# Kernel tuning notes

Hardware: AMD Instinct MI355X
Metric: run time of the kernel (lower is better)

## Reference

```python
import jax, jax.numpy as jnp
import numpy as np

IMAGE_W = 640.0
IMAGE_H = 640.0
ALPHA = 0.25
GAMMA = 2.0
BETA = 1.0 / 9.0
EPS = 1e-4
FACTOR = jnp.array([0.1, 0.1, 0.2, 0.2], dtype=jnp.float32)

B, A, C, M = 8, 76725, 80, 20


def _iou(anchors, gts):
    # anchors [A,4], gts [M,4] -> [A,M]
    lt = jnp.maximum(anchors[:, None, :2], gts[None, :, :2])
    rb = jnp.minimum(anchors[:, None, 2:], gts[None, :, 2:])
    wh = jnp.clip(rb - lt, 0.0)
    inter = wh[..., 0] * wh[..., 1]
    area_a = (anchors[:, 2] - anchors[:, 0]) * (anchors[:, 3] - anchors[:, 1])
    area_g = (gts[:, 2] - gts[:, 0]) * (gts[:, 3] - gts[:, 1])
    union = area_a[:, None] + area_g[None, :] - inter
    return inter / jnp.maximum(union, 1e-6)


def _snap(gt_boxes, anchors):
    # xyxy -> (tx,ty,tw,th)/factor
    awh = anchors[:, 2:] - anchors[:, :2]
    actr = anchors[:, :2] + 0.5 * awh
    gwh = jnp.maximum(gt_boxes[:, 2:] - gt_boxes[:, :2], 1.0)
    gctr = gt_boxes[:, :2] + 0.5 * gwh
    t = jnp.concatenate([(gctr - actr) / awh, jnp.log(gwh / awh)], axis=1)
    return t / FACTOR


def _assign(anchors, ann):
    # anchors [A,4], ann [M,5] -> boxes [A,4], cls [A]
    valid = ann[:, 4] >= 0.0
    gt_boxes, gt_cls = ann[:, :4], ann[:, 4]
    ious = jnp.where(valid[None, :], _iou(anchors, gt_boxes), -1.0)
    idx = jnp.argmax(ious, axis=1)
    overlap = jnp.take_along_axis(ious, idx[:, None], axis=1)[:, 0]
    boxes = _snap(gt_boxes[idx], anchors)
    cls = jnp.full_like(overlap, -1.0)
    cls = jnp.where(overlap < 0.4, 0.0, cls)
    cls = jnp.where(overlap >= 0.5, gt_cls[idx] + 1.0, cls)
    cls = jnp.where(jnp.any(valid), cls, -1.0)  # no gt: all ignore
    return boxes, cls


def setup_inputs() -> dict:
    key = jax.random.key(0)
    k1, k2, k3, k4, k5, k6, k7 = jax.random.split(key, 7)
    ctr = jax.random.uniform(k1, (B, A, 2), minval=0.0, maxval=640.0)
    wh = jax.random.uniform(k2, (B, A, 2), minval=16.0, maxval=256.0)
    batch_anchors = jnp.concatenate([ctr - 0.5 * wh, ctr + 0.5 * wh], axis=-1)
    cls_heads = jax.random.uniform(k3, (B, A, C), minval=0.01, maxval=0.99)
    reg_heads = jax.random.normal(k4, (B, A, 4)) * 0.1
    xy = jax.random.uniform(k5, (B, M, 2), minval=0.0, maxval=480.0)
    gwh = jax.random.uniform(k6, (B, M, 2), minval=32.0, maxval=160.0)
    gcls = jax.random.randint(k7, (B, M), 0, C).astype(jnp.float32)
    gcls = gcls.at[:, 15:].set(-1.0)  # pad slots
    annotations = jnp.concatenate([xy, xy + gwh, gcls[..., None]], axis=-1)
    return {"cls_heads": cls_heads, "reg_heads": reg_heads,
            "batch_anchors": batch_anchors, "annotations": annotations}


def reference(cls_heads, reg_heads, batch_anchors, annotations):
    # border filter (original drops rows; we mask -> same loss)
    border = ((batch_anchors[..., 0] > 0.0) & (batch_anchors[..., 1] > 0.0) &
              (batch_anchors[..., 2] < IMAGE_W) & (batch_anchors[..., 3] < IMAGE_H))
    boxes, cls = jax.vmap(_assign)(batch_anchors, annotations)  # [B,A,4],[B,A]
    cls = jnp.where(border, cls, -1.0)
    pos = cls > 0.0
    keep = cls >= 0.0
    pos_num = jnp.sum(pos, axis=1)  # [B]
    valid_img = pos_num > 0
    safe_pos = jnp.maximum(pos_num, 1).astype(cls_heads.dtype)

    # focal (cls) loss
    p = jnp.clip(cls_heads, EPS, 1.0 - EPS)
    gt = jax.nn.one_hot(cls.astype(jnp.int32), C + 1, dtype=p.dtype)[..., 1:]
    af = jnp.where(gt == 1.0, ALPHA, 1.0 - ALPHA)
    pt = jnp.where(gt == 1.0, p, 1.0 - p)
    bce = -(gt * jnp.log(p) + (1.0 - gt) * jnp.log(1.0 - p))
    focal = af * (1.0 - pt) ** GAMMA * bce
    per_img_cls = jnp.sum(focal * keep[..., None].astype(p.dtype), axis=(1, 2)) / safe_pos
    per_img_cls = jnp.where(valid_img, per_img_cls, 0.0)

    # smooth-L1 (reg) loss
    x = jnp.abs(reg_heads - boxes)
    sl1 = jnp.where(x >= BETA, x - 0.5 * BETA, 0.5 * x * x / BETA).mean(axis=2)
    per_img_reg = jnp.sum(sl1 * pos.astype(sl1.dtype), axis=1) / safe_pos
    per_img_reg = jnp.where(valid_img, per_img_reg, 0.0)

    n = jnp.maximum(jnp.sum(valid_img), 1).astype(per_img_cls.dtype)
    return per_img_cls.sum() / n, per_img_reg.sum() / n
```

## Files before the change

kernel.cpp:

```cpp
#include <hip/hip_runtime.h>
#include <math.h>

#define B_CNT 8
#define A_CNT 76725
#define C_CNT 80
#define M_CNT 20

constexpr int XR = (A_CNT + 255) / 256;
constexpr int XC = 512;
constexpr int NG = (A_CNT + 15) / 16;

__global__ __launch_bounds__(256) void assign_kernel(
    const float* __restrict__ anchors,
    const float* __restrict__ reg_heads,
    const float* __restrict__ ann,
    float* __restrict__ cls_out,
    double* __restrict__ partial_reg,
    int* __restrict__ partial_pos)
{
    __shared__ float s_ann[M_CNT * 5];
    const int b   = blockIdx.y;
    const int tid = threadIdx.x;
    if (tid < M_CNT * 5) s_ann[tid] = ann[b * M_CNT * 5 + tid];
    __syncthreads();

    const int a = blockIdx.x * 256 + tid;
    double slsum = 0.0;
    int pos = 0;

    if (a < A_CNT) {
        const float4 ab = ((const float4*)anchors)[b * A_CNT + a];
        const float ax1 = ab.x, ay1 = ab.y, ax2 = ab.z, ay2 = ab.w;
        const bool border = (ax1 > 0.0f) && (ay1 > 0.0f) &&
                            (ax2 < 640.0f) && (ay2 < 640.0f);
        const float area_a = (ax2 - ax1) * (ay2 - ay1);

        float best = -INFINITY;
        int   bi   = 0;
        bool  anyv = false;
        #pragma unroll
        for (int m = 0; m < M_CNT; ++m) {
            const float gx1 = s_ann[m * 5 + 0];
            const float gy1 = s_ann[m * 5 + 1];
            const float gx2 = s_ann[m * 5 + 2];
            const float gy2 = s_ann[m * 5 + 3];
            const float gc  = s_ann[m * 5 + 4];
            const bool v = (gc >= 0.0f);
            anyv = anyv || v;
            const float ltx = fmaxf(ax1, gx1), lty = fmaxf(ay1, gy1);
            const float rbx = fminf(ax2, gx2), rby = fminf(ay2, gy2);
            const float wx = fmaxf(rbx - ltx, 0.0f);
            const float wy = fmaxf(rby - lty, 0.0f);
            const float inter = wx * wy;
            const float area_g = (gx2 - gx1) * (gy2 - gy1);
            const float uni = area_a + area_g - inter;
            const float iou = v ? (inter / fmaxf(uni, 1e-6f)) : -1.0f;
            if (iou > best) { best = iou; bi = m; }
        }

        float clsv = -1.0f;
        if (anyv) {
            if (best < 0.4f)       clsv = 0.0f;
            else if (best >= 0.5f) clsv = s_ann[bi * 5 + 4] + 1.0f;
        }
        if (!border) clsv = -1.0f;
        cls_out[b * A_CNT + a] = clsv;

        if (clsv > 0.0f) {
            pos = 1;
            const float gx1 = s_ann[bi * 5 + 0];
            const float gy1 = s_ann[bi * 5 + 1];
            const float gx2 = s_ann[bi * 5 + 2];
            const float gy2 = s_ann[bi * 5 + 3];
            const float aw = ax2 - ax1, ah = ay2 - ay1;
            const float acx = ax1 + 0.5f * aw, acy = ay1 + 0.5f * ah;
            const float gw = fmaxf(gx2 - gx1, 1.0f);
            const float gh = fmaxf(gy2 - gy1, 1.0f);
            const float gcx = gx1 + 0.5f * gw, gcy = gy1 + 0.5f * gh;
            const float t0 = ((gcx - acx) / aw) / 0.1f;
            const float t1 = ((gcy - acy) / ah) / 0.1f;
            const float t2 = logf(gw / aw) / 0.2f;
            const float t3 = logf(gh / ah) / 0.2f;
            const float4 rh = ((const float4*)reg_heads)[b * A_CNT + a];

            const float BETA = (float)(1.0 / 9.0);
            const float HB   = (float)(0.5 * (1.0 / 9.0));
            auto sl1 = [&](float x) {
                x = fabsf(x);
                return (x >= BETA) ? (x - HB) : (0.5f * x * x / BETA);
            };
            const float s = (sl1(rh.x - t0) + sl1(rh.y - t1) +
                             sl1(rh.z - t2) + sl1(rh.w - t3)) * 0.25f;
            slsum = (double)s;
        }
    }

    for (int o = 32; o; o >>= 1) {
        slsum += __shfl_down(slsum, o);
        pos   += __shfl_down(pos, o);
    }
    __shared__ double sd[4];
    __shared__ int    si[4];
    const int w = tid >> 6;
    if ((tid & 63) == 0) { sd[w] = slsum; si[w] = pos; }
    __syncthreads();
    if (tid == 0) {
        partial_reg[b * XR + blockIdx.x] = sd[0] + sd[1] + sd[2] + sd[3];
        partial_pos[b * XR + blockIdx.x] = si[0] + si[1] + si[2] + si[3];
    }
}

__global__ __launch_bounds__(320) void focal_kernel(
    const float* __restrict__ cls_heads,
    const float* __restrict__ cls_f,
    double* __restrict__ partial_cls)
{
    const int b   = blockIdx.y;
    const int tid = threadIdx.x;
    const int la  = tid / 20;
    const int c0  = (tid % 20) * 4;

    double acc = 0.0;
    for (int g = blockIdx.x; g < NG; g += XC) {
        const int a = g * 16 + la;
        if (a >= A_CNT) continue;
        const float clsv = cls_f[b * A_CNT + a];
        if (clsv < 0.0f) continue;
        const int gidx = (int)clsv - 1;

        const float4 p4 = *((const float4*)(
            cls_heads + ((size_t)b * A_CNT + (size_t)a) * C_CNT + c0));
        const float pp[4] = {p4.x, p4.y, p4.z, p4.w};

        float lacc = 0.0f;
        #pragma unroll
        for (int j = 0; j < 4; ++j) {
            const float p   = fminf(fmaxf(pp[j], 1e-4f), 0.9999f);
            const float omp = 1.0f - p;
            const bool  isgt = (c0 + j) == gidx;
            const float q  = isgt ? omp : (1.0f - omp);
            const float af = isgt ? 0.25f : 0.75f;
            const float x  = isgt ? p : omp;
            lacc += af * (q * q) * (-__logf(x));
        }
        acc += (double)lacc;
    }

    for (int o = 32; o; o >>= 1) acc += __shfl_down(acc, o);
    __shared__ double sd[5];
    if ((tid & 63) == 0) sd[tid >> 6] = acc;
    __syncthreads();
    if (tid == 0)
        partial_cls[b * XC + blockIdx.x] = sd[0] + sd[1] + sd[2] + sd[3] + sd[4];
}

__global__ __launch_bounds__(256) void finalize_kernel(
    const double* __restrict__ partial_cls,
    const double* __restrict__ partial_reg,
    const int* __restrict__ partial_pos,
    float* __restrict__ out)
{
    const int tid = threadIdx.x;
    __shared__ double sc[4], sr[4];
    __shared__ int    sp[4];

    double cls_tot = 0.0, reg_tot = 0.0;
    int nv = 0;

    for (int b = 0; b < B_CNT; ++b) {
        double cs = 0.0;
        for (int i = tid; i < XC; i += 256) cs += partial_cls[b * XC + i];
        double rs = 0.0;
        int    ps = 0;
        for (int i = tid; i < XR; i += 256) {
            rs += partial_reg[b * XR + i];
            ps += partial_pos[b * XR + i];
        }
        for (int o = 32; o; o >>= 1) {
            cs += __shfl_down(cs, o);
            rs += __shfl_down(rs, o);
            ps += __shfl_down(ps, o);
        }
        const int w = tid >> 6;
        if ((tid & 63) == 0) { sc[w] = cs; sr[w] = rs; sp[w] = ps; }
        __syncthreads();
        if (tid == 0) {
            const double c = sc[0] + sc[1] + sc[2] + sc[3];
            const double r = sr[0] + sr[1] + sr[2] + sr[3];
            const int    p = sp[0] + sp[1] + sp[2] + sp[3];
            if (p > 0) { cls_tot += c / (double)p; reg_tot += r / (double)p; ++nv; }
        }
        __syncthreads();
    }

    if (tid == 0) {
        const int n = (nv > 0) ? nv : 1;
        out[0] = (float)(cls_tot / (double)n);
        out[1] = (float)(reg_tot / (double)n);
    }
}

extern "C" void kernel_launch(void* const* d_in, const int* in_sizes, int n_in,
                              void* d_out, int out_size, void* d_ws, size_t ws_size,
                              hipStream_t stream) {
    const float* cls_heads = (const float*)d_in[0];
    const float* reg_heads = (const float*)d_in[1];
    const float* anchors   = (const float*)d_in[2];
    const float* ann       = (const float*)d_in[3];
    float* out = (float*)d_out;

    char* ws = (char*)d_ws;
    double* partial_cls = (double*)ws;
    double* partial_reg = (double*)(ws + 32768);
    int*    partial_pos = (int*)(ws + 32768 + 19200);
    float*  cls_f       = (float*)(ws + 32768 + 19200 + 9600);

    assign_kernel<<<dim3(XR, B_CNT), 256, 0, stream>>>(
        anchors, reg_heads, ann, cls_f, partial_reg, partial_pos);
    focal_kernel<<<dim3(XC, B_CNT), 320, 0, stream>>>(
        cls_heads, cls_f, partial_cls);
    finalize_kernel<<<1, 256, 0, stream>>>(
        partial_cls, partial_reg, partial_pos, out);
}
```

Measured before the change: 305.1 us.

## Fuse anchor assignment and focal loss into one per-block kernel

Merges the assignment kernel and the focal-loss kernel into one kernel. Each 256-anchor block computes its anchors' labels, keeps them in shared memory, then streams the matching contiguous cls_heads slab (256×80 floats) and adds its focal loss. This drops the global round trip of the per-anchor label array and one kernel launch. It also replaces the grid-stride focal loop with many blocks that each read a contiguous slab, and merges all three partial reductions into one pass. The cost is that the focal work now waits on the IoU loop within each block, and the block shape is fixed at 256 anchors.

```diff
diff --git a/kernel.cpp b/kernel.cpp
--- a/kernel.cpp
+++ b/kernel.cpp
@@ -7,26 +7,29 @@
 #define M_CNT 20
 
 constexpr int XR = (A_CNT + 255) / 256;
-constexpr int XC = 512;
-constexpr int NG = (A_CNT + 15) / 16;
-
-__global__ __launch_bounds__(256) void assign_kernel(
+
+__global__ __launch_bounds__(256) void fused_kernel(
+    const float* __restrict__ cls_heads,
+    const float* __restrict__ reg_heads,
     const float* __restrict__ anchors,
-    const float* __restrict__ reg_heads,
     const float* __restrict__ ann,
-    float* __restrict__ cls_out,
+    double* __restrict__ partial_cls,
     double* __restrict__ partial_reg,
     int* __restrict__ partial_pos)
 {
     __shared__ float s_ann[M_CNT * 5];
+    __shared__ float s_cls[256];
     const int b   = blockIdx.y;
     const int tid = threadIdx.x;
     if (tid < M_CNT * 5) s_ann[tid] = ann[b * M_CNT * 5 + tid];
     __syncthreads();
 
-    const int a = blockIdx.x * 256 + tid;
+    const int a0 = blockIdx.x * 256;
+    const int a  = a0 + tid;
+
     double slsum = 0.0;
-    int pos = 0;
+    int    pos   = 0;
+    float  clsv  = -1.0f;
 
     if (a < A_CNT) {
         const float4 ab = ((const float4*)anchors)[b * A_CNT + a];
@@ -58,13 +61,11 @@
             if (iou > best) { best = iou; bi = m; }
         }
 
-        float clsv = -1.0f;
         if (anyv) {
             if (best < 0.4f)       clsv = 0.0f;
             else if (best >= 0.5f) clsv = s_ann[bi * 5 + 4] + 1.0f;
         }
         if (!border) clsv = -1.0f;
-        cls_out[b * A_CNT + a] = clsv;
 
         if (clsv > 0.0f) {
             pos = 1;
@@ -94,42 +95,21 @@
             slsum = (double)s;
         }
     }
-
-    for (int o = 32; o; o >>= 1) {
-        slsum += __shfl_down(slsum, o);
-        pos   += __shfl_down(pos, o);
-    }
-    __shared__ double sd[4];
-    __shared__ int    si[4];
-    const int w = tid >> 6;
-    if ((tid & 63) == 0) { sd[w] = slsum; si[w] = pos; }
+    s_cls[tid] = clsv;
     __syncthreads();
-    if (tid == 0) {
-        partial_reg[b * XR + blockIdx.x] = sd[0] + sd[1] + sd[2] + sd[3];
-        partial_pos[b * XR + blockIdx.x] = si[0] + si[1] + si[2] + si[3];
-    }
-}
-
-__global__ __launch_bounds__(320) void focal_kernel(
-    const float* __restrict__ cls_heads,
-    const float* __restrict__ cls_f,
-    double* __restrict__ partial_cls)
-{
-    const int b   = blockIdx.y;
-    const int tid = threadIdx.x;
-    const int la  = tid / 20;
-    const int c0  = (tid % 20) * 4;
-
+
+    const float* slab = cls_heads + ((size_t)b * A_CNT + (size_t)a0) * C_CNT;
     double acc = 0.0;
-    for (int g = blockIdx.x; g < NG; g += XC) {
-        const int a = g * 16 + la;
-        if (a >= A_CNT) continue;
-        const float clsv = cls_f[b * A_CNT + a];
-        if (clsv < 0.0f) continue;
-        const int gidx = (int)clsv - 1;
-
-        const float4 p4 = *((const float4*)(
-            cls_heads + ((size_t)b * A_CNT + (size_t)a) * C_CNT + c0));
+    #pragma unroll 4
+    for (int i = 0; i < 20; ++i) {
+        const int idx = tid + (i << 8);
+        const int la  = idx / 20;
+        const int c0  = (idx - la * 20) * 4;
+        const float cv = s_cls[la];
+        if (cv < 0.0f) continue;
+        const int gidx = (int)cv - 1;
+
+        const float4 p4 = *((const float4*)(slab + (size_t)la * C_CNT + c0));
         const float pp[4] = {p4.x, p4.y, p4.z, p4.w};
 
         float lacc = 0.0f;
@@ -146,12 +126,21 @@
         acc += (double)lacc;
     }
 
-    for (int o = 32; o; o >>= 1) acc += __shfl_down(acc, o);
-    __shared__ double sd[5];
-    if ((tid & 63) == 0) sd[tid >> 6] = acc;
+    for (int o = 32; o; o >>= 1) {
+        acc   += __shfl_down(acc, o);
+        slsum += __shfl_down(slsum, o);
+        pos   += __shfl_down(pos, o);
+    }
+    __shared__ double sdc[4], sdr[4];
+    __shared__ int    sip[4];
+    const int w = tid >> 6;
+    if ((tid & 63) == 0) { sdc[w] = acc; sdr[w] = slsum; sip[w] = pos; }
     __syncthreads();
-    if (tid == 0)
-        partial_cls[b * XC + blockIdx.x] = sd[0] + sd[1] + sd[2] + sd[3] + sd[4];
+    if (tid == 0) {
+        partial_cls[b * XR + blockIdx.x] = sdc[0] + sdc[1] + sdc[2] + sdc[3];
+        partial_reg[b * XR + blockIdx.x] = sdr[0] + sdr[1] + sdr[2] + sdr[3];
+        partial_pos[b * XR + blockIdx.x] = sip[0] + sip[1] + sip[2] + sip[3];
+    }
 }
 
 __global__ __launch_bounds__(256) void finalize_kernel(
@@ -168,11 +157,10 @@
     int nv = 0;
 
     for (int b = 0; b < B_CNT; ++b) {
-        double cs = 0.0;
-        for (int i = tid; i < XC; i += 256) cs += partial_cls[b * XC + i];
-        double rs = 0.0;
+        double cs = 0.0, rs = 0.0;
         int    ps = 0;
         for (int i = tid; i < XR; i += 256) {
+            cs += partial_cls[b * XR + i];
             rs += partial_reg[b * XR + i];
             ps += partial_pos[b * XR + i];
         }
@@ -211,14 +199,12 @@
 
     char* ws = (char*)d_ws;
     double* partial_cls = (double*)ws;
-    double* partial_reg = (double*)(ws + 32768);
-    int*    partial_pos = (int*)(ws + 32768 + 19200);
-    float*  cls_f       = (float*)(ws + 32768 + 19200 + 9600);
-
-    assign_kernel<<<dim3(XR, B_CNT), 256, 0, stream>>>(
-        anchors, reg_heads, ann, cls_f, partial_reg, partial_pos);
-    focal_kernel<<<dim3(XC, B_CNT), 320, 0, stream>>>(
-        cls_heads, cls_f, partial_cls);
+    double* partial_reg = (double*)(ws + 19200);
+    int*    partial_pos = (int*)(ws + 38400);
+
+    fused_kernel<<<dim3(XR, B_CNT), 256, 0, stream>>>(
+        cls_heads, reg_heads, anchors, ann,
+        partial_cls, partial_reg, partial_pos);
     finalize_kernel<<<1, 256, 0, stream>>>(
         partial_cls, partial_reg, partial_pos, out);
 }
```

Result: faster. 290.2 us (-4.9%).
